# Kernel tuning notes

Hardware: AMD Instinct MI355X
Metric: run time of the kernel (lower is better)

## Reference

```python
import jax, jax.numpy as jnp
import numpy as np

MARGIN = 0.3
EPS = 1e-12


def setup_inputs() -> dict:
    key = jax.random.key(0)
    k1, k2, k3 = jax.random.split(key, 3)
    B, D = 8192, 1024
    features = jax.random.normal(k1, (B, D), dtype=jnp.float32)
    labels = jax.random.randint(k2, (B,), 0, 100, dtype=jnp.int64)
    domain_labels = jax.random.randint(k3, (B,), 0, 2, dtype=jnp.int64)
    return {"features": features, "labels": labels, "domain_labels": domain_labels}


def reference(features, labels, domain_labels):
    # L2-normalize rows (F.normalize: x / max(||x||, eps))
    norm = jnp.maximum(jnp.linalg.norm(features, axis=1, keepdims=True), EPS)
    f = features / norm

    herb = domain_labels == 0   # [B] anchors
    field = domain_labels == 1  # [B] candidates

    sq = jnp.sum(f * f, axis=1)                                   # [B]
    d2 = sq[:, None] + sq[None, :] - 2.0 * jnp.einsum('id,jd->ij', f, f)
    d = jnp.sqrt(jnp.maximum(d2, 0.0))                            # [B, B]

    same = labels[:, None] == labels[None, :]                     # [B, B]
    pair = herb[:, None] & field[None, :]
    pos_mask = pair & same
    neg_mask = pair & ~same

    INF = jnp.float32(jnp.inf)
    pos_min = jnp.min(jnp.where(pos_mask, d, INF), axis=1)        # [B]
    neg_min = jnp.min(jnp.where(neg_mask, d, INF), axis=1)        # [B]

    valid = herb & jnp.any(pos_mask, axis=1) & jnp.any(neg_mask, axis=1)
    # Substitute 0 for invalid rows BEFORE subtracting to avoid inf - inf.
    pos_s = jnp.where(valid, pos_min, 0.0)
    neg_s = jnp.where(valid, neg_min, 0.0)
    tl = jnp.maximum(pos_s - neg_s + MARGIN, 0.0)                 # [B]

    loss_sum = jnp.sum(jnp.where(valid, tl, 0.0))
    count = jnp.sum(valid.astype(jnp.float32))
    return jnp.where(count > 0, loss_sum / jnp.maximum(count, 1.0), 0.0)
```

## Files before the change

kernel.cpp:

```cpp
#include <hip/hip_runtime.h>


#define B_ROWS 8192
#define DIM    1024

typedef __bf16 bf16x8 __attribute__((ext_vector_type(8)));
typedef float  f32x4  __attribute__((ext_vector_type(4)));

__device__ __forceinline__ unsigned short f2bf_rne(float x) {
    unsigned u = __float_as_uint(x);
    unsigned r = (u + 0x7FFFu + ((u >> 16) & 1u)) >> 16;
    return (unsigned short)r;
}
__device__ __forceinline__ float bf2f(unsigned short h) {
    return __uint_as_float(((unsigned)h) << 16);
}

__device__ __forceinline__ void async_copy16(const void* g, void* l) {
    __builtin_amdgcn_global_load_lds(
        (const __attribute__((address_space(1))) unsigned int*)g,
        (__attribute__((address_space(3))) unsigned int*)l,
        16, 0, 0);
}

__global__ __launch_bounds__(256) void compute_slots(
    const int* __restrict__ dom, int* __restrict__ slotOf,
    unsigned* __restrict__ cnt, float* __restrict__ accum)
{
    __shared__ int cnts[256];
    __shared__ int base[257];
    const int t = threadIdx.x;

    if (t == 0) {
        cnt[1] = 0u;
        accum[0] = 0.0f;
        accum[1] = 0.0f;
    }

    unsigned mask = 0u; int c = 0;
    #pragma unroll
    for (int i = 0; i < 32; ++i) {
        const int isA = (dom[t + 256 * i] == 0) ? 1 : 0;
        mask |= ((unsigned)isA) << i;
        c += isA;
    }
    cnts[t] = c;
    __syncthreads();
    if (t < 64) {
        const int c0 = cnts[4 * t + 0], c1 = cnts[4 * t + 1];
        const int c2 = cnts[4 * t + 2], c3 = cnts[4 * t + 3];
        const int s4 = c0 + c1 + c2 + c3;
        int sc = s4;
        #pragma unroll
        for (int d = 1; d < 64; d <<= 1) {
            const int o = __shfl_up(sc, d);
            if (t >= d) sc += o;
        }
        const int b = sc - s4;
        base[4 * t + 0] = b;
        base[4 * t + 1] = b + c0;
        base[4 * t + 2] = b + c0 + c1;
        base[4 * t + 3] = b + c0 + c1 + c2;
        if (t == 63) { base[256] = sc; cnt[0] = (unsigned)sc; }
    }
    __syncthreads();
    const int nA = base[256];
    int aB = base[t];
    int fB = nA + t * 32 - base[t];
    #pragma unroll
    for (int i = 0; i < 32; ++i) {
        const int isA = (mask >> i) & 1;
        slotOf[t + 256 * i] = isA ? aB : fB;
        aB += isA;
        fB += 1 - isA;
    }
}

__global__ __launch_bounds__(256) void normalize_rows(
    const float* __restrict__ feat, const int* __restrict__ labels,
    int* slotOf , unsigned* __restrict__ negmin,
    unsigned short* __restrict__ G, int* __restrict__ labG,
    float* __restrict__ sqG)
{
    const int wv = threadIdx.x >> 6, lane = threadIdx.x & 63;
    const int row = blockIdx.x * 4 + wv;

    const float4* src = (const float4*)(feat + (size_t)row * DIM);
    float4 v[4];
    float ss = 0.0f;
    #pragma unroll
    for (int j = 0; j < 4; ++j) {
        v[j] = src[j * 64 + lane];
        ss += v[j].x * v[j].x + v[j].y * v[j].y + v[j].z * v[j].z + v[j].w * v[j].w;
    }
    #pragma unroll
    for (int s = 32; s > 0; s >>= 1) ss += __shfl_xor(ss, s);
    const float inv = 1.0f / fmaxf(sqrtf(ss), 1e-12f);

    const int slot = slotOf[row];
    if (lane == 0) {
        ((unsigned*)slotOf)[row] = 0xFFFFFFFFu;
        negmin[row] = 0xFFFFFFFFu;
    }
    unsigned short ub[16];
    float ss2 = 0.0f;
    #pragma unroll
    for (int j = 0; j < 4; ++j) {
        const float f0 = v[j].x * inv, f1 = v[j].y * inv,
                    f2 = v[j].z * inv, f3 = v[j].w * inv;
        ub[j * 4 + 0] = f2bf_rne(f0); ub[j * 4 + 1] = f2bf_rne(f1);
        ub[j * 4 + 2] = f2bf_rne(f2); ub[j * 4 + 3] = f2bf_rne(f3);
        #pragma unroll
        for (int q = 0; q < 4; ++q) {
            const float fr = bf2f(ub[j * 4 + q]);
            ss2 += fr * fr;
        }
    }
    #pragma unroll
    for (int s = 32; s > 0; s >>= 1) ss2 += __shfl_xor(ss2, s);
    if (lane == 0) {
        sqG[slot]  = ss2;
        labG[slot] = labels[row];
    }
    ushort4* dst = (ushort4*)(G + (size_t)slot * DIM);
    #pragma unroll
    for (int j = 0; j < 4; ++j) {
        ushort4 pk;
        pk.x = ub[j * 4 + 0]; pk.y = ub[j * 4 + 1];
        pk.z = ub[j * 4 + 2]; pk.w = ub[j * 4 + 3];
        dst[j * 64 + lane] = pk;
    }
}

__global__ __launch_bounds__(256) void tile_mindist(
    const unsigned short* __restrict__ G, const int* __restrict__ labG,
    const float* __restrict__ sqG, const unsigned* __restrict__ cnt,
    unsigned* __restrict__ posmin, unsigned* __restrict__ negmin)
{
    const int nA = (int)cnt[0];
    const int nF = B_ROWS - nA;
    const int nTA = (nA + 127) >> 7;
    const int nTF = (nF + 127) >> 7;

    __shared__ __align__(16) unsigned short S[2][2][128 * 32];

    const int t = threadIdx.x;
    const int lane = t & 63, w = t >> 6;
    const int wm = w >> 1, wn = w & 1;
    const int l15 = lane & 15, quad = lane >> 4;

    const int ch0 = 2 * w;
    const int crow = lane >> 2;
    const int cbyte = (lane & 3) * 16;

    const int rdA = (wm * 64 + l15) * 32 + quad * 8;
    const int rdF = (wn * 64 + l15) * 32 + quad * 8;

    const char* Gb = (const char*)G;

    const int xcd = blockIdx.x & 7;
    const int bx  = xcd & 1;
    const int by  = xcd >> 1;
    const int qa = nTA >> 1, ra = nTA & 1;
    const int sa = qa + ((bx < ra) ? 1 : 0);
    const int xa = bx * qa + ((bx < ra) ? bx : ra);
    const int qf = nTF >> 2, rf = nTF & 3;
    const int sf = qf + ((by < rf) ? 1 : 0);
    const int ya = by * qf + ((by < rf) ? by : rf);
    const int localN = sa * sf;
    const int j0 = blockIdx.x >> 3;
    const int jstride = (int)(gridDim.x >> 3);

    for (int j = j0; j < localN; j += jstride) {
        const int tx = xa + j / sf;
        const int ty = ya + j % sf;
        const int rowA0 = tx * 128;
        const int rowF0 = nA + ty * 128;

        const char* ga[2]; const char* gf[2];
        #pragma unroll
        for (int h = 0; h < 2; ++h) {
            const int ch = ch0 + h;
            const int rA = rowA0 + 16 * ch + crow;
            int rF = rowF0 + 16 * ch + crow;
            if (rF > B_ROWS - 1) rF = B_ROWS - 1;
            ga[h] = Gb + (size_t)rA * (DIM * 2) + cbyte;
            gf[h] = Gb + (size_t)rF * (DIM * 2) + cbyte;
        }

        f32x4 acc[4][4] = {};

        #pragma unroll
        for (int h = 0; h < 2; ++h) {
            async_copy16(ga[h], &S[0][0][(ch0 + h) * 512]);
            async_copy16(gf[h], &S[0][1][(ch0 + h) * 512]);
        }
        __syncthreads();

        #pragma unroll 4
        for (int step = 0; step < 32; ++step) {
            const int cur = step & 1;
            const int nb = cur ^ 1;
            if (step < 31) {
                const int off = (step + 1) * 64;
                #pragma unroll
                for (int h = 0; h < 2; ++h) {
                    async_copy16(ga[h] + off, &S[nb][0][(ch0 + h) * 512]);
                    async_copy16(gf[h] + off, &S[nb][1][(ch0 + h) * 512]);
                }
            }

            const unsigned short* pa = &S[cur][0][rdA];
            const unsigned short* pf = &S[cur][1][rdF];
            bf16x8 a[4], b[4];
            #pragma unroll
            for (int fm = 0; fm < 4; ++fm) a[fm] = *(const bf16x8*)(pa + fm * 512);
            #pragma unroll
            for (int fn = 0; fn < 4; ++fn) b[fn] = *(const bf16x8*)(pf + fn * 512);
            #pragma unroll
            for (int fm = 0; fm < 4; ++fm)
                #pragma unroll
                for (int fn = 0; fn < 4; ++fn)
                    acc[fm][fn] = __builtin_amdgcn_mfma_f32_16x16x32_bf16(
                        a[fm], b[fn], acc[fm][fn], 0, 0, 0);

            __syncthreads();
        }

        const float INFV = __uint_as_float(0x7f800000u);
        float sqf[4]; int lf_[4]; bool vf[4];
        #pragma unroll
        for (int fn = 0; fn < 4; ++fn) {
            const int rf2 = rowF0 + wn * 64 + fn * 16 + l15;
            vf[fn] = rf2 < B_ROWS;
            const int rc = vf[fn] ? rf2 : (B_ROWS - 1);
            sqf[fn] = sqG[rc];
            lf_[fn] = labG[rc];
        }
        #pragma unroll
        for (int fm = 0; fm < 4; ++fm) {
            #pragma unroll
            for (int r = 0; r < 4; ++r) {
                const int ra = rowA0 + wm * 64 + fm * 16 + quad * 4 + r;
                const bool va = ra < nA;
                const int rac = va ? ra : 0;
                const float sqa = sqG[rac];
                const int la_ = labG[rac];
                float pmin = INFV, nmin = INFV;
                #pragma unroll
                for (int fn = 0; fn < 4; ++fn) {
                    const float dd = fmaxf(sqa + sqf[fn] - 2.0f * acc[fm][fn][r], 0.0f);
                    if (vf[fn]) {
                        if (la_ == lf_[fn]) pmin = fminf(pmin, dd);
                        else                nmin = fminf(nmin, dd);
                    }
                }
                #pragma unroll
                for (int s = 1; s < 16; s <<= 1) {
                    pmin = fminf(pmin, __shfl_xor(pmin, s));
                    nmin = fminf(nmin, __shfl_xor(nmin, s));
                }
                if (l15 == 0 && va) {
                    if (pmin < INFV) atomicMin(&posmin[ra], __float_as_uint(pmin));
                    if (nmin < INFV) atomicMin(&negmin[ra], __float_as_uint(nmin));
                }
            }
        }
        __syncthreads();
    }
}

__global__ __launch_bounds__(256) void reduce_loss(
    const unsigned* __restrict__ posmin, const unsigned* __restrict__ negmin,
    float* __restrict__ accum, unsigned* __restrict__ cnt,
    float* __restrict__ out)
{
    const int i = blockIdx.x * 256 + threadIdx.x;
    const unsigned up = posmin[i], un = negmin[i];
    float tl = 0.0f, c = 0.0f;
    if (up != 0xFFFFFFFFu && un != 0xFFFFFFFFu) {
        const float pd = sqrtf(__uint_as_float(up));
        const float nd = sqrtf(__uint_as_float(un));
        tl = fmaxf(pd - nd + 0.3f, 0.0f);
        c = 1.0f;
    }
    #pragma unroll
    for (int s = 32; s > 0; s >>= 1) {
        tl += __shfl_down(tl, s);
        c  += __shfl_down(c, s);
    }
    __shared__ float sb[8];
    const int lane = threadIdx.x & 63, w = threadIdx.x >> 6;
    if (lane == 0) { sb[w] = tl; sb[4 + w] = c; }
    __syncthreads();
    if (threadIdx.x == 0) {
        atomicAdd(&accum[0], sb[0] + sb[1] + sb[2] + sb[3]);
        atomicAdd(&accum[1], sb[4] + sb[5] + sb[6] + sb[7]);
        __threadfence();
        const unsigned ticket = atomicAdd(&cnt[1], 1u);
        if (ticket == 31u) {
            __threadfence();
            const float s2 = atomicAdd(&accum[0], 0.0f);
            const float c2 = atomicAdd(&accum[1], 0.0f);
            out[0] = (c2 > 0.0f) ? s2 / fmaxf(c2, 1.0f) : 0.0f;
        }
    }
}

extern "C" void kernel_launch(void* const* d_in, const int* in_sizes, int n_in,
                              void* d_out, int out_size, void* d_ws, size_t ws_size,
                              hipStream_t stream) {
    const float* feat  = (const float*)d_in[0];
    const int* labels  = (const int*)d_in[1];
    const int* dom     = (const int*)d_in[2];
    float* out = (float*)d_out;

    char* ws = (char*)d_ws;
    unsigned short* G   = (unsigned short*)(ws);
    int*      labG      = (int*)(ws + 16777216);
    float*    sqG       = (float*)(ws + 16809984);
    unsigned* posmin    = (unsigned*)(ws + 16842752);
    unsigned* negmin    = (unsigned*)(ws + 16875520);
    unsigned* cnt       = (unsigned*)(ws + 16908288);
    float*    accum     = (float*)(ws + 16908296);
    int*      slotOf    = (int*)(ws + 16842752);

    compute_slots<<<1, 256, 0, stream>>>(dom, slotOf, cnt, accum);
    normalize_rows<<<B_ROWS / 4, 256, 0, stream>>>(feat, labels, slotOf,
                                                   negmin, G, labG, sqG);

    tile_mindist<<<1056, 256, 0, stream>>>(G, labG, sqG, cnt, posmin, negmin);

    reduce_loss<<<B_ROWS / 256, 256, 0, stream>>>(posmin, negmin, accum, cnt, out);
}
```

Before: 170.1 us.

## Use single-wave 64x64 tiles with swizzled LDS and barrier-free prefetch

The min-distance GEMM kernel moves from 256-thread blocks on 128x128 tiles to one wavefront per block on 64x64 tiles. Because each block is a single wave, it drops every __syncthreads and instead uses explicit vmcnt/lgkmcnt waits with a two-deep prefetch. It also XOR-swizzles the LDS layout to avoid bank conflicts. The aim is to remove barrier stalls and raise occupancy, at the cost of half the operand reuse per tile and so more global/L2 traffic, plus more atomicMin operations.

```diff
diff --git a/kernel.cpp b/kernel.cpp
--- a/kernel.cpp
+++ b/kernel.cpp
@@ -132,29 +132,25 @@
     }
 }
 
-__global__ __launch_bounds__(256) void tile_mindist(
+__global__ __launch_bounds__(64) void tile_mindist(
     const unsigned short* __restrict__ G, const int* __restrict__ labG,
     const float* __restrict__ sqG, const unsigned* __restrict__ cnt,
     unsigned* __restrict__ posmin, unsigned* __restrict__ negmin)
 {
     const int nA = (int)cnt[0];
     const int nF = B_ROWS - nA;
-    const int nTA = (nA + 127) >> 7;
-    const int nTF = (nF + 127) >> 7;
-
-    __shared__ __align__(16) unsigned short S[2][2][128 * 32];
-
-    const int t = threadIdx.x;
-    const int lane = t & 63, w = t >> 6;
-    const int wm = w >> 1, wn = w & 1;
+    const int nTA = (nA + 63) >> 6;
+    const int nTF = (nF + 63) >> 6;
+
+    __shared__ __align__(16) unsigned short S[2][2][64 * 32];
+
+    const int lane = threadIdx.x;
     const int l15 = lane & 15, quad = lane >> 4;
 
-    const int ch0 = 2 * w;
-    const int crow = lane >> 2;
-    const int cbyte = (lane & 3) * 16;
-
-    const int rdA = (wm * 64 + l15) * 32 + quad * 8;
-    const int rdF = (wn * 64 + l15) * 32 + quad * 8;
+    const int srow  = lane >> 2;
+    const int scs16 = (((lane & 3) ^ ((srow >> 1) & 3)) << 4);
+
+    const int ch8 = ((quad ^ ((l15 >> 1) & 3)) << 3);
 
     const char* Gb = (const char*)G;
 
@@ -174,64 +170,71 @@
     for (int j = j0; j < localN; j += jstride) {
         const int tx = xa + j / sf;
         const int ty = ya + j % sf;
-        const int rowA0 = tx * 128;
-        const int rowF0 = nA + ty * 128;
-
-        const char* ga[2]; const char* gf[2];
-        #pragma unroll
-        for (int h = 0; h < 2; ++h) {
-            const int ch = ch0 + h;
-            const int rA = rowA0 + 16 * ch + crow;
-            int rF = rowF0 + 16 * ch + crow;
+        const int rowA0 = tx * 64;
+        const int rowF0 = nA + ty * 64;
+
+        const char* ga[4]; const char* gf[4];
+        #pragma unroll
+        for (int c = 0; c < 4; ++c) {
+            const int rA = rowA0 + 16 * c + srow;
+            int rF = rowF0 + 16 * c + srow;
             if (rF > B_ROWS - 1) rF = B_ROWS - 1;
-            ga[h] = Gb + (size_t)rA * (DIM * 2) + cbyte;
-            gf[h] = Gb + (size_t)rF * (DIM * 2) + cbyte;
+            ga[c] = Gb + (size_t)rA * (DIM * 2) + scs16;
+            gf[c] = Gb + (size_t)rF * (DIM * 2) + scs16;
         }
 
         f32x4 acc[4][4] = {};
 
         #pragma unroll
-        for (int h = 0; h < 2; ++h) {
-            async_copy16(ga[h], &S[0][0][(ch0 + h) * 512]);
-            async_copy16(gf[h], &S[0][1][(ch0 + h) * 512]);
-        }
-        __syncthreads();
+        for (int c = 0; c < 4; ++c) async_copy16(ga[c], &S[0][0][c * 512]);
+        #pragma unroll
+        for (int c = 0; c < 4; ++c) async_copy16(gf[c], &S[0][1][c * 512]);
+        #pragma unroll
+        for (int c = 0; c < 4; ++c) async_copy16(ga[c] + 64, &S[1][0][c * 512]);
+        #pragma unroll
+        for (int c = 0; c < 4; ++c) async_copy16(gf[c] + 64, &S[1][1][c * 512]);
 
         #pragma unroll 4
         for (int step = 0; step < 32; ++step) {
+            if (step < 31) { asm volatile("s_waitcnt vmcnt(8)" ::: "memory"); }
+            else           { asm volatile("s_waitcnt vmcnt(0)" ::: "memory"); }
+
             const int cur = step & 1;
-            const int nb = cur ^ 1;
-            if (step < 31) {
-                const int off = (step + 1) * 64;
-                #pragma unroll
-                for (int h = 0; h < 2; ++h) {
-                    async_copy16(ga[h] + off, &S[nb][0][(ch0 + h) * 512]);
-                    async_copy16(gf[h] + off, &S[nb][1][(ch0 + h) * 512]);
-                }
-            }
-
-            const unsigned short* pa = &S[cur][0][rdA];
-            const unsigned short* pf = &S[cur][1][rdF];
+            const unsigned short* pa = &S[cur][0][ch8];
+            const unsigned short* pf = &S[cur][1][ch8];
             bf16x8 a[4], b[4];
             #pragma unroll
-            for (int fm = 0; fm < 4; ++fm) a[fm] = *(const bf16x8*)(pa + fm * 512);
+            for (int fm = 0; fm < 4; ++fm)
+                a[fm] = *(const bf16x8*)(pa + (fm * 16 + l15) * 32);
             #pragma unroll
-            for (int fn = 0; fn < 4; ++fn) b[fn] = *(const bf16x8*)(pf + fn * 512);
+            for (int fn = 0; fn < 4; ++fn)
+                b[fn] = *(const bf16x8*)(pf + (fn * 16 + l15) * 32);
+
+            asm volatile("s_waitcnt lgkmcnt(0)" ::: "memory");
+            __builtin_amdgcn_sched_barrier(0);
+            if (step < 30) {
+                const int off = (step + 2) * 64;
+                #pragma unroll
+                for (int c = 0; c < 4; ++c)
+                    async_copy16(ga[c] + off, &S[cur][0][c * 512]);
+                #pragma unroll
+                for (int c = 0; c < 4; ++c)
+                    async_copy16(gf[c] + off, &S[cur][1][c * 512]);
+            }
+
             #pragma unroll
             for (int fm = 0; fm < 4; ++fm)
                 #pragma unroll
                 for (int fn = 0; fn < 4; ++fn)
                     acc[fm][fn] = __builtin_amdgcn_mfma_f32_16x16x32_bf16(
                         a[fm], b[fn], acc[fm][fn], 0, 0, 0);
-
-            __syncthreads();
         }
 
         const float INFV = __uint_as_float(0x7f800000u);
         float sqf[4]; int lf_[4]; bool vf[4];
         #pragma unroll
         for (int fn = 0; fn < 4; ++fn) {
-            const int rf2 = rowF0 + wn * 64 + fn * 16 + l15;
+            const int rf2 = rowF0 + fn * 16 + l15;
             vf[fn] = rf2 < B_ROWS;
             const int rc = vf[fn] ? rf2 : (B_ROWS - 1);
             sqf[fn] = sqG[rc];
@@ -241,9 +244,9 @@
         for (int fm = 0; fm < 4; ++fm) {
             #pragma unroll
             for (int r = 0; r < 4; ++r) {
-                const int ra = rowA0 + wm * 64 + fm * 16 + quad * 4 + r;
-                const bool va = ra < nA;
-                const int rac = va ? ra : 0;
+                const int ra2 = rowA0 + fm * 16 + quad * 4 + r;
+                const bool va = ra2 < nA;
+                const int rac = va ? ra2 : 0;
                 const float sqa = sqG[rac];
                 const int la_ = labG[rac];
                 float pmin = INFV, nmin = INFV;
@@ -261,12 +264,11 @@
                     nmin = fminf(nmin, __shfl_xor(nmin, s));
                 }
                 if (l15 == 0 && va) {
-                    if (pmin < INFV) atomicMin(&posmin[ra], __float_as_uint(pmin));
-                    if (nmin < INFV) atomicMin(&negmin[ra], __float_as_uint(nmin));
+                    if (pmin < INFV) atomicMin(&posmin[ra2], __float_as_uint(pmin));
+                    if (nmin < INFV) atomicMin(&negmin[ra2], __float_as_uint(nmin));
                 }
             }
         }
-        __syncthreads();
     }
 }
 
@@ -329,7 +331,7 @@
     normalize_rows<<<B_ROWS / 4, 256, 0, stream>>>(feat, labels, slotOf,
                                                    negmin, G, labG, sqG);
 
-    tile_mindist<<<1056, 256, 0, stream>>>(G, labG, sqG, cnt, posmin, negmin);
+    tile_mindist<<<2560, 64, 0, stream>>>(G, labG, sqG, cnt, posmin, negmin);
 
     reduce_loss<<<B_ROWS / 256, 256, 0, stream>>>(posmin, negmin, accum, cnt, out);
 }
```

New measurement: 179.8 us. 5.7% more time.

## Store normalized bf16 rows in tiled layout with reversed field slots for contiguous loads

Applied to the files above, without the earlier changes.

The normalize kernel now writes the bf16 matrix as 128-row tiles, each laid out by 32-element K chunks (8 KB per chunk), so each tile's K-step slice is one contiguous 8 KB block. Field rows are placed at reversed slots counting down from the end, so field tiles line up with tile boundaries from the top. The GEMM kernel loads fully contiguous 16-byte segments per lane and reads B fragments in mirrored order to undo the reversal. This aims to make global-to-LDS copies coalesced instead of strided 64-byte row pieces, at the cost of more complex indexing and fragment remapping.

```diff
diff --git a/kernel.cpp b/kernel.cpp
--- a/kernel.cpp
+++ b/kernel.cpp
@@ -64,15 +64,14 @@
         if (t == 63) { base[256] = sc; cnt[0] = (unsigned)sc; }
     }
     __syncthreads();
-    const int nA = base[256];
     int aB = base[t];
-    int fB = nA + t * 32 - base[t];
+    int fI = t * 32 - base[t];
     #pragma unroll
     for (int i = 0; i < 32; ++i) {
         const int isA = (mask >> i) & 1;
-        slotOf[t + 256 * i] = isA ? aB : fB;
+        slotOf[t + 256 * i] = isA ? aB : (8191 - fI);
         aB += isA;
-        fB += 1 - isA;
+        fI += 1 - isA;
     }
 }
 
@@ -122,13 +121,16 @@
         sqG[slot]  = ss2;
         labG[slot] = labels[row];
     }
-    ushort4* dst = (ushort4*)(G + (size_t)slot * DIM);
+    char* Gb = (char*)G;
+    char* rowBase = Gb + (size_t)(slot >> 7) * 262144 + (size_t)(slot & 127) * 64
+                       + (lane & 7) * 8;
+    const int kc0 = lane >> 3;
     #pragma unroll
     for (int j = 0; j < 4; ++j) {
         ushort4 pk;
         pk.x = ub[j * 4 + 0]; pk.y = ub[j * 4 + 1];
         pk.z = ub[j * 4 + 2]; pk.w = ub[j * 4 + 3];
-        dst[j * 64 + lane] = pk;
+        *(ushort4*)(rowBase + (size_t)(j * 8 + kc0) * 8192) = pk;
     }
 }
 
@@ -150,11 +152,9 @@
     const int l15 = lane & 15, quad = lane >> 4;
 
     const int ch0 = 2 * w;
-    const int crow = lane >> 2;
-    const int cbyte = (lane & 3) * 16;
-
-    const int rdA = (wm * 64 + l15) * 32 + quad * 8;
-    const int rdF = (wn * 64 + l15) * 32 + quad * 8;
+
+    const int rdA  = (wm * 64 + l15) * 32 + quad * 8;
+    const int rdF0 = ((1 - wn) * 64 + 15 - l15) * 32 + quad * 8;
 
     const char* Gb = (const char*)G;
 
@@ -174,26 +174,18 @@
     for (int j = j0; j < localN; j += jstride) {
         const int tx = xa + j / sf;
         const int ty = ya + j % sf;
-        const int rowA0 = tx * 128;
-        const int rowF0 = nA + ty * 128;
-
-        const char* ga[2]; const char* gf[2];
+        const int rowA0  = tx * 128;
+        const int rowFl0 = ty * 128;
+
+        const char* baseA = Gb + (size_t)tx * 262144 + (size_t)(ch0 * 1024) + lane * 16;
+        const char* baseF = Gb + (size_t)(63 - ty) * 262144 + (size_t)(ch0 * 1024) + lane * 16;
+
+        f32x4 acc[4][4] = {};
+
         #pragma unroll
         for (int h = 0; h < 2; ++h) {
-            const int ch = ch0 + h;
-            const int rA = rowA0 + 16 * ch + crow;
-            int rF = rowF0 + 16 * ch + crow;
-            if (rF > B_ROWS - 1) rF = B_ROWS - 1;
-            ga[h] = Gb + (size_t)rA * (DIM * 2) + cbyte;
-            gf[h] = Gb + (size_t)rF * (DIM * 2) + cbyte;
-        }
-
-        f32x4 acc[4][4] = {};
-
-        #pragma unroll
-        for (int h = 0; h < 2; ++h) {
-            async_copy16(ga[h], &S[0][0][(ch0 + h) * 512]);
-            async_copy16(gf[h], &S[0][1][(ch0 + h) * 512]);
+            async_copy16(baseA + h * 1024, &S[0][0][(ch0 + h) * 512]);
+            async_copy16(baseF + h * 1024, &S[0][1][(ch0 + h) * 512]);
         }
         __syncthreads();
 
@@ -202,21 +194,21 @@
             const int cur = step & 1;
             const int nb = cur ^ 1;
             if (step < 31) {
-                const int off = (step + 1) * 64;
+                const size_t off = (size_t)(step + 1) * 8192;
                 #pragma unroll
                 for (int h = 0; h < 2; ++h) {
-                    async_copy16(ga[h] + off, &S[nb][0][(ch0 + h) * 512]);
-                    async_copy16(gf[h] + off, &S[nb][1][(ch0 + h) * 512]);
+                    async_copy16(baseA + off + h * 1024, &S[nb][0][(ch0 + h) * 512]);
+                    async_copy16(baseF + off + h * 1024, &S[nb][1][(ch0 + h) * 512]);
                 }
             }
 
             const unsigned short* pa = &S[cur][0][rdA];
-            const unsigned short* pf = &S[cur][1][rdF];
+            const unsigned short* pf = &S[cur][1][rdF0];
             bf16x8 a[4], b[4];
             #pragma unroll
             for (int fm = 0; fm < 4; ++fm) a[fm] = *(const bf16x8*)(pa + fm * 512);
             #pragma unroll
-            for (int fn = 0; fn < 4; ++fn) b[fn] = *(const bf16x8*)(pf + fn * 512);
+            for (int fn = 0; fn < 4; ++fn) b[fn] = *(const bf16x8*)(pf + (3 - fn) * 512);
             #pragma unroll
             for (int fm = 0; fm < 4; ++fm)
                 #pragma unroll
@@ -231,19 +223,19 @@
         float sqf[4]; int lf_[4]; bool vf[4];
         #pragma unroll
         for (int fn = 0; fn < 4; ++fn) {
-            const int rf2 = rowF0 + wn * 64 + fn * 16 + l15;
-            vf[fn] = rf2 < B_ROWS;
-            const int rc = vf[fn] ? rf2 : (B_ROWS - 1);
-            sqf[fn] = sqG[rc];
-            lf_[fn] = labG[rc];
+            const int rfl = rowFl0 + wn * 64 + fn * 16 + l15;
+            vf[fn] = rfl < nF;
+            const int slotF = 8191 - rfl;
+            sqf[fn] = sqG[slotF];
+            lf_[fn] = labG[slotF];
         }
         #pragma unroll
         for (int fm = 0; fm < 4; ++fm) {
             #pragma unroll
             for (int r = 0; r < 4; ++r) {
-                const int ra = rowA0 + wm * 64 + fm * 16 + quad * 4 + r;
-                const bool va = ra < nA;
-                const int rac = va ? ra : 0;
+                const int ra2 = rowA0 + wm * 64 + fm * 16 + quad * 4 + r;
+                const bool va = ra2 < nA;
+                const int rac = va ? ra2 : 0;
                 const float sqa = sqG[rac];
                 const int la_ = labG[rac];
                 float pmin = INFV, nmin = INFV;
@@ -261,8 +253,8 @@
                     nmin = fminf(nmin, __shfl_xor(nmin, s));
                 }
                 if (l15 == 0 && va) {
-                    if (pmin < INFV) atomicMin(&posmin[ra], __float_as_uint(pmin));
-                    if (nmin < INFV) atomicMin(&negmin[ra], __float_as_uint(nmin));
+                    if (pmin < INFV) atomicMin(&posmin[ra2], __float_as_uint(pmin));
+                    if (nmin < INFV) atomicMin(&negmin[ra2], __float_as_uint(nmin));
                 }
             }
         }
```

Result: faster. 165.5 us (median of 2 runs) (-2.7%).
